# Kernel tuning notes

Measured on AMD Instinct MI355X. Metric: run time of the kernel, lower is better.

## Reference

```python
import jax, jax.numpy as jnp
import numpy as np

EPS = 1e-5  # BatchNorm eps


def _bn_relu(x, g, b, m, v):
    # inference-mode BatchNorm2d over channel axis 1, then ReLU
    inv = g / jnp.sqrt(v + EPS)
    return jax.nn.relu(x * inv[None, :, None, None] + (b - m * inv)[None, :, None, None])


def setup_inputs() -> dict:
    key = jax.random.key(0)
    ks = jax.random.split(key, 16)
    B, C, N, K = 8, 64, 16384, 16
    mlp = (128, 64, 64)
    inp = {
        "src_xyz": jax.random.normal(ks[0], (B, 3, N, K), jnp.float32),
        "tgt_xyz": jax.random.normal(ks[1], (B, 3, N), jnp.float32),
        "feature": jax.random.normal(ks[2], (B, C, N, K), jnp.float32),
    }
    prev = C + 4  # use_relation adds diff_xyz(3) + distance(1)
    i = 3
    for li, co in enumerate(mlp, 1):
        scale = (6.0 / (prev + co)) ** 0.5  # xavier_uniform
        inp[f"W{li}"] = jax.random.uniform(ks[i], (co, prev), jnp.float32, -scale, scale)
        inp[f"g{li}"] = jnp.ones((co,), jnp.float32)
        inp[f"b{li}"] = jnp.zeros((co,), jnp.float32)
        inp[f"m{li}"] = jnp.zeros((co,), jnp.float32)
        inp[f"v{li}"] = jnp.ones((co,), jnp.float32)
        prev = co
        i += 1
    return inp


def reference(src_xyz, tgt_xyz, feature,
              W1, g1, b1, m1, v1,
              W2, g2, b2, m2, v2,
              W3, g3, b3, m3, v3):
    d = 3  # NOTE: original code slices the NEIGHBOR dim to :3 (faithful quirk)
    diff = src_xyz[:, :, :, :d] - tgt_xyz[:, :, :, None]      # (B,3,N,3)
    dist = jnp.sum(diff * diff, axis=1, keepdims=True)        # (B,1,N,3)
    x = jnp.concatenate([feature[:, :, :, :d], diff, dist], axis=1)  # (B,C+4,N,3)
    for (W, g, b, m, v) in ((W1, g1, b1, m1, v1), (W2, g2, b2, m2, v2), (W3, g3, b3, m3, v3)):
        x = jnp.einsum('oc,bcnk->bonk', W, x)  # 1x1 conv (shared MLP)
        x = _bn_relu(x, g, b, m, v)
    return jnp.sum(x, axis=3)  # reduction='sum' over neighbor dim -> (B,64,N)
```

## Files before the change

### kernel.cpp

```cpp
#include <hip/hip_runtime.h>


typedef __attribute__((ext_vector_type(8))) short short8v;
typedef __attribute__((ext_vector_type(4))) float f32x4;

#define BN_EPS 1e-5f

__device__ __forceinline__ unsigned short f2bf(float f) {
    union { float f; unsigned u; } U; U.f = f;
    unsigned r = U.u + 0x7FFFu + ((U.u >> 16) & 1u);
    return (unsigned short)(r >> 16);
}

union FragU { uint4 u; short8v s; uint2 h[2]; };


__global__ __launch_bounds__(256) void fa_pack(
    const float* __restrict__ W1, const float* __restrict__ g1, const float* __restrict__ b1,
    const float* __restrict__ m1, const float* __restrict__ v1,
    const float* __restrict__ W2, const float* __restrict__ g2, const float* __restrict__ b2,
    const float* __restrict__ m2, const float* __restrict__ v2,
    const float* __restrict__ W3, const float* __restrict__ g3, const float* __restrict__ b3,
    const float* __restrict__ m3, const float* __restrict__ v3,
    char* __restrict__ ws)
{
    const int id = blockIdx.x * 256 + threadIdx.x;
    if (id < 1536) {
        const int lane = id & 63, frag = id >> 6;
        const int ct = frag / 3, ks = frag - 3 * ct;
        const int o  = ct * 16 + (lane & 15);
        const int kb = ks * 32 + (lane >> 4) * 8;
        unsigned short h[8];
        #pragma unroll
        for (int j = 0; j < 8; ++j) {
            const int k = kb + j;
            h[j] = (k < 68) ? f2bf(W1[o * 68 + k]) : (unsigned short)0;
        }
        uint4 pk;
        pk.x = h[0] | (h[1] << 16); pk.y = h[2] | (h[3] << 16);
        pk.z = h[4] | (h[5] << 16); pk.w = h[6] | (h[7] << 16);
        ((uint4*)ws)[id] = pk;
    } else if (id < 2560) {
        const int i2 = id - 1536;
        const int lane = i2 & 63, frag = i2 >> 6;
        const int o  = (frag >> 2) * 16 + (lane & 15);
        const int kb = (frag & 3) * 32 + (lane >> 4) * 8;
        unsigned short h[8];
        #pragma unroll
        for (int j = 0; j < 8; ++j) h[j] = f2bf(W2[o * 128 + kb + j]);
        uint4 pk;
        pk.x = h[0] | (h[1] << 16); pk.y = h[2] | (h[3] << 16);
        pk.z = h[4] | (h[5] << 16); pk.w = h[6] | (h[7] << 16);
        ((uint4*)(ws + 24576))[i2] = pk;
    } else if (id < 3072) {
        const int i3 = id - 2560;
        const int lane = i3 & 63, frag = i3 >> 6;
        const int o  = (frag >> 1) * 16 + (lane & 15);
        const int kb = (frag & 1) * 32 + (lane >> 4) * 8;
        unsigned short h[8];
        #pragma unroll
        for (int j = 0; j < 8; ++j) h[j] = f2bf(W3[o * 64 + kb + j]);
        uint4 pk;
        pk.x = h[0] | (h[1] << 16); pk.y = h[2] | (h[3] << 16);
        pk.z = h[4] | (h[5] << 16); pk.w = h[6] | (h[7] << 16);
        ((uint4*)(ws + 40960))[i3] = pk;
    } else if (id < 3200) {
        const int o = id - 3072;
        const float s = g1[o] * rsqrtf(v1[o] + BN_EPS);
        ((float*)(ws + 49152))[o] = s;
        ((float*)(ws + 49664))[o] = b1[o] - m1[o] * s;
    } else if (id < 3264) {
        const int o = id - 3200;
        const float s = g2[o] * rsqrtf(v2[o] + BN_EPS);
        ((float*)(ws + 50176))[o] = s;
        ((float*)(ws + 50432))[o] = b2[o] - m2[o] * s;
    } else if (id < 3328) {
        const int o = id - 3264;
        const float s = g3[o] * rsqrtf(v3[o] + BN_EPS);
        ((float*)(ws + 50688))[o] = s;
        ((float*)(ws + 50944))[o] = b3[o] - m3[o] * s;
    }
}

__global__ __launch_bounds__(128, 2) void fa_mfma(
    const float* __restrict__ src, const float* __restrict__ tgt,
    const float* __restrict__ feat,
    const char* __restrict__ ws, float* __restrict__ out)
{
    constexpr int N = 16384;
    __shared__ unsigned short X0[96 * 72];
    __shared__ unsigned short X1[96 * 136];

    const int t  = threadIdx.x;
    const int b  = blockIdx.x >> 9;
    const int n0 = (blockIdx.x & 511) << 5;

    {
        const int p  = t & 31;
        const int cg = t >> 5;
        #pragma unroll
        for (int it = 0; it < 4; ++it) {
            const int c0 = it * 16 + cg * 4;
            const float* fp = feat + ((size_t)(b * 64 + c0) * N + n0 + p) * 16;
            const float4 f0 = *(const float4*)(fp);
            const float4 f1 = *(const float4*)(fp + (size_t)N * 16);
            const float4 f2 = *(const float4*)(fp + (size_t)N * 32);
            const float4 f3 = *(const float4*)(fp + (size_t)N * 48);
            uint2 u0, u1, u2;
            u0.x = f2bf(f0.x) | (f2bf(f1.x) << 16); u0.y = f2bf(f2.x) | (f2bf(f3.x) << 16);
            u1.x = f2bf(f0.y) | (f2bf(f1.y) << 16); u1.y = f2bf(f2.y) | (f2bf(f3.y) << 16);
            u2.x = f2bf(f0.z) | (f2bf(f1.z) << 16); u2.y = f2bf(f2.z) | (f2bf(f3.z) << 16);
            *(uint2*)&X0[(0 * 32 + p) * 72 + c0] = u0;
            *(uint2*)&X0[(1 * 32 + p) * 72 + c0] = u1;
            *(uint2*)&X0[(2 * 32 + p) * 72 + c0] = u2;
        }
    }
    if (t < 96) {
        const int p = t & 31, k = t >> 5;
        const int n = n0 + p;
        const float d0 = src[((b * 3 + 0) * N + n) * 16 + k] - tgt[(b * 3 + 0) * N + n];
        const float d1 = src[((b * 3 + 1) * N + n) * 16 + k] - tgt[(b * 3 + 1) * N + n];
        const float d2 = src[((b * 3 + 2) * N + n) * 16 + k] - tgt[(b * 3 + 2) * N + n];
        const float ds = d0 * d0 + d1 * d1 + d2 * d2;
        uint2 wr; wr.x = f2bf(d0) | (f2bf(d1) << 16); wr.y = f2bf(d2) | (f2bf(ds) << 16);
        *(uint2*)&X0[(k * 32 + p) * 72 + 64] = wr;
        uint2 z; z.x = 0; z.y = 0;
        *(uint2*)&X0[(k * 32 + p) * 72 + 68] = z;
    }
    __syncthreads();

    const int w = t >> 6, lane = t & 63, lo = lane & 15, hi = lane >> 4;

    const uint4*  w1f = (const uint4*)ws;
    const uint4*  w2f = (const uint4*)(ws + 24576);
    const uint4*  w3f = (const uint4*)(ws + 40960);
    const float*  s1w = (const float*)(ws + 49152);
    const float*  t1w = (const float*)(ws + 49664);
    const float*  s2w = (const float*)(ws + 50176);
    const float*  t2w = (const float*)(ws + 50432);
    const float*  s3w = (const float*)(ws + 50688);
    const float*  t3w = (const float*)(ws + 50944);

    short8v a1[3][3];
    #pragma unroll
    for (int k = 0; k < 3; ++k) {
        const int row = k * 32 + w * 16 + lo;
        a1[k][0] = *(const short8v*)&X0[row * 72 + hi * 8];
        a1[k][1] = *(const short8v*)&X0[row * 72 + 32 + hi * 8];
        short8v az = {0, 0, 0, 0, 0, 0, 0, 0};
        if (hi == 0) {
            FragU U; U.s = az;
            U.h[0] = *(const uint2*)&X0[row * 72 + 64];
            az = U.s;
        }
        a1[k][2] = az;
    }
    #pragma unroll 2
    for (int ct = 0; ct < 8; ++ct) {
        FragU B0, B1, B2;
        B0.u = w1f[(ct * 3 + 0) * 64 + lane];
        B1.u = w1f[(ct * 3 + 1) * 64 + lane];
        B2.u = w1f[(ct * 3 + 2) * 64 + lane];
        const float sc = s1w[ct * 16 + lo];
        const float tb = t1w[ct * 16 + lo];
        #pragma unroll
        for (int k = 0; k < 3; ++k) {
            f32x4 acc = {0.f, 0.f, 0.f, 0.f};
            acc = __builtin_amdgcn_mfma_f32_16x16x32_bf16(a1[k][0], B0.s, acc, 0, 0, 0);
            acc = __builtin_amdgcn_mfma_f32_16x16x32_bf16(a1[k][1], B1.s, acc, 0, 0, 0);
            acc = __builtin_amdgcn_mfma_f32_16x16x32_bf16(a1[k][2], B2.s, acc, 0, 0, 0);
            const int rb = k * 32 + w * 16 + 4 * hi;
            #pragma unroll
            for (int j = 0; j < 4; ++j) {
                const float y = fmaxf(fmaf(sc, acc[j], tb), 0.f);
                X1[(rb + j) * 136 + ct * 16 + lo] = f2bf(y);
            }
        }
    }

    short8v a2[3][4];
    #pragma unroll
    for (int k = 0; k < 3; ++k) {
        const int row = k * 32 + w * 16 + lo;
        #pragma unroll
        for (int ks = 0; ks < 4; ++ks)
            a2[k][ks] = *(const short8v*)&X1[row * 136 + ks * 32 + hi * 8];
    }
    #pragma unroll 2
    for (int ct = 0; ct < 4; ++ct) {
        FragU B0, B1, B2, B3;
        B0.u = w2f[(ct * 4 + 0) * 64 + lane];
        B1.u = w2f[(ct * 4 + 1) * 64 + lane];
        B2.u = w2f[(ct * 4 + 2) * 64 + lane];
        B3.u = w2f[(ct * 4 + 3) * 64 + lane];
        const float sc = s2w[ct * 16 + lo];
        const float tb = t2w[ct * 16 + lo];
        #pragma unroll
        for (int k = 0; k < 3; ++k) {
            f32x4 acc = {0.f, 0.f, 0.f, 0.f};
            acc = __builtin_amdgcn_mfma_f32_16x16x32_bf16(a2[k][0], B0.s, acc, 0, 0, 0);
            acc = __builtin_amdgcn_mfma_f32_16x16x32_bf16(a2[k][1], B1.s, acc, 0, 0, 0);
            acc = __builtin_amdgcn_mfma_f32_16x16x32_bf16(a2[k][2], B2.s, acc, 0, 0, 0);
            acc = __builtin_amdgcn_mfma_f32_16x16x32_bf16(a2[k][3], B3.s, acc, 0, 0, 0);
            const int rb = k * 32 + w * 16 + 4 * hi;
            #pragma unroll
            for (int j = 0; j < 4; ++j) {
                const float y = fmaxf(fmaf(sc, acc[j], tb), 0.f);
                X0[(rb + j) * 72 + ct * 16 + lo] = f2bf(y);
            }
        }
    }

    short8v a3[3][2];
    #pragma unroll
    for (int k = 0; k < 3; ++k) {
        const int row = k * 32 + w * 16 + lo;
        a3[k][0] = *(const short8v*)&X0[row * 72 + hi * 8];
        a3[k][1] = *(const short8v*)&X0[row * 72 + 32 + hi * 8];
    }
    #pragma unroll 2
    for (int ct = 0; ct < 4; ++ct) {
        FragU B0, B1;
        B0.u = w3f[(ct * 2 + 0) * 64 + lane];
        B1.u = w3f[(ct * 2 + 1) * 64 + lane];
        const float sc = s3w[ct * 16 + lo];
        const float tb = t3w[ct * 16 + lo];
        f32x4 acc0 = {0.f, 0.f, 0.f, 0.f};
        f32x4 acc1 = {0.f, 0.f, 0.f, 0.f};
        f32x4 acc2 = {0.f, 0.f, 0.f, 0.f};
        acc0 = __builtin_amdgcn_mfma_f32_16x16x32_bf16(a3[0][0], B0.s, acc0, 0, 0, 0);
        acc0 = __builtin_amdgcn_mfma_f32_16x16x32_bf16(a3[0][1], B1.s, acc0, 0, 0, 0);
        acc1 = __builtin_amdgcn_mfma_f32_16x16x32_bf16(a3[1][0], B0.s, acc1, 0, 0, 0);
        acc1 = __builtin_amdgcn_mfma_f32_16x16x32_bf16(a3[1][1], B1.s, acc1, 0, 0, 0);
        acc2 = __builtin_amdgcn_mfma_f32_16x16x32_bf16(a3[2][0], B0.s, acc2, 0, 0, 0);
        acc2 = __builtin_amdgcn_mfma_f32_16x16x32_bf16(a3[2][1], B1.s, acc2, 0, 0, 0);
        float4 r;
        float* rp = &r.x;
        #pragma unroll
        for (int j = 0; j < 4; ++j) {
            rp[j] = fmaxf(fmaf(sc, acc0[j], tb), 0.f)
                  + fmaxf(fmaf(sc, acc1[j], tb), 0.f)
                  + fmaxf(fmaf(sc, acc2[j], tb), 0.f);
        }
        float* op = out + (size_t)(b * 64 + ct * 16 + lo) * N + n0 + w * 16 + 4 * hi;
        *(float4*)op = r;
    }
}

extern "C" void kernel_launch(void* const* d_in, const int* in_sizes, int n_in,
                              void* d_out, int out_size, void* d_ws, size_t ws_size,
                              hipStream_t stream)
{
    const float* src  = (const float*)d_in[0];
    const float* tgt  = (const float*)d_in[1];
    const float* feat = (const float*)d_in[2];
    const float* W1 = (const float*)d_in[3];
    const float* g1 = (const float*)d_in[4];
    const float* b1 = (const float*)d_in[5];
    const float* m1 = (const float*)d_in[6];
    const float* v1 = (const float*)d_in[7];
    const float* W2 = (const float*)d_in[8];
    const float* g2 = (const float*)d_in[9];
    const float* b2 = (const float*)d_in[10];
    const float* m2 = (const float*)d_in[11];
    const float* v2 = (const float*)d_in[12];
    const float* W3 = (const float*)d_in[13];
    const float* g3 = (const float*)d_in[14];
    const float* b3 = (const float*)d_in[15];
    const float* m3 = (const float*)d_in[16];
    const float* v3 = (const float*)d_in[17];
    float* out = (float*)d_out;
    char* ws = (char*)d_ws;

    hipLaunchKernelGGL(fa_pack, dim3(13), dim3(256), 0, stream,
                       W1, g1, b1, m1, v1, W2, g2, b2, m2, v2, W3, g3, b3, m3, v3, ws);
    hipLaunchKernelGGL(fa_mfma, dim3(8 * 512), dim3(128), 0, stream,
                       src, tgt, feat, ws, out);
}
```

Measured before the change: 144.1 us.

## Alias LDS buffers, batch global loads up front, raise occupancy to three blocks

The two shared-memory staging buffers are merged into one aliased array, with extra barriers so each layer's fragments are read into registers before the buffer is overwritten. This cuts LDS use per block. The launch bound is raised to ask for three blocks per SIMD. All 16 feature float4 loads and the src/tgt loads are now issued before any conversion, to expose more memory-level parallelism. The trade-offs are higher register pressure from the 16 buffered float4 values, which may conflict with the tighter register budget, and two added block-wide barriers. The zero padding write at column 68 is also dropped, since those entries are never read.

```diff
diff --git a/kernel.cpp b/kernel.cpp
--- a/kernel.cpp
+++ b/kernel.cpp
@@ -82,14 +82,15 @@
     }
 }
 
-__global__ __launch_bounds__(128, 2) void fa_mfma(
+__global__ __launch_bounds__(128, 3) void fa_mfma(
     const float* __restrict__ src, const float* __restrict__ tgt,
     const float* __restrict__ feat,
     const char* __restrict__ ws, float* __restrict__ out)
 {
     constexpr int N = 16384;
-    __shared__ unsigned short X0[96 * 72];
-    __shared__ unsigned short X1[96 * 136];
+    __shared__ unsigned short SM[96 * 136];
+    #define X0V(r, c) SM[(r) * 72 + (c)]
+    #define X1V(r, c) SM[(r) * 136 + (c)]
 
     const int t  = threadIdx.x;
     const int b  = blockIdx.x >> 9;
@@ -98,34 +99,42 @@
     {
         const int p  = t & 31;
         const int cg = t >> 5;
+        float4 fr[16];
+        #pragma unroll
+        for (int it = 0; it < 4; ++it) {
+            const float* fp = feat + ((size_t)(b * 64 + it * 16 + cg * 4) * N + n0 + p) * 16;
+            #pragma unroll
+            for (int q = 0; q < 4; ++q)
+                fr[it * 4 + q] = *(const float4*)(fp + (size_t)q * N * 16);
+        }
+        float rs0 = 0, rs1 = 0, rs2 = 0, rt0 = 0, rt1 = 0, rt2 = 0;
+        const bool rel = t < 96;
+        const int rp = t & 31, rk = t >> 5;
+        if (rel) {
+            const int n = n0 + rp;
+            rs0 = src[((b * 3 + 0) * N + n) * 16 + rk]; rt0 = tgt[(b * 3 + 0) * N + n];
+            rs1 = src[((b * 3 + 1) * N + n) * 16 + rk]; rt1 = tgt[(b * 3 + 1) * N + n];
+            rs2 = src[((b * 3 + 2) * N + n) * 16 + rk]; rt2 = tgt[(b * 3 + 2) * N + n];
+        }
         #pragma unroll
         for (int it = 0; it < 4; ++it) {
             const int c0 = it * 16 + cg * 4;
-            const float* fp = feat + ((size_t)(b * 64 + c0) * N + n0 + p) * 16;
-            const float4 f0 = *(const float4*)(fp);
-            const float4 f1 = *(const float4*)(fp + (size_t)N * 16);
-            const float4 f2 = *(const float4*)(fp + (size_t)N * 32);
-            const float4 f3 = *(const float4*)(fp + (size_t)N * 48);
+            const float4 f0 = fr[it * 4 + 0], f1 = fr[it * 4 + 1];
+            const float4 f2 = fr[it * 4 + 2], f3 = fr[it * 4 + 3];
             uint2 u0, u1, u2;
             u0.x = f2bf(f0.x) | (f2bf(f1.x) << 16); u0.y = f2bf(f2.x) | (f2bf(f3.x) << 16);
             u1.x = f2bf(f0.y) | (f2bf(f1.y) << 16); u1.y = f2bf(f2.y) | (f2bf(f3.y) << 16);
             u2.x = f2bf(f0.z) | (f2bf(f1.z) << 16); u2.y = f2bf(f2.z) | (f2bf(f3.z) << 16);
-            *(uint2*)&X0[(0 * 32 + p) * 72 + c0] = u0;
-            *(uint2*)&X0[(1 * 32 + p) * 72 + c0] = u1;
-            *(uint2*)&X0[(2 * 32 + p) * 72 + c0] = u2;
-        }
-    }
-    if (t < 96) {
-        const int p = t & 31, k = t >> 5;
-        const int n = n0 + p;
-        const float d0 = src[((b * 3 + 0) * N + n) * 16 + k] - tgt[(b * 3 + 0) * N + n];
-        const float d1 = src[((b * 3 + 1) * N + n) * 16 + k] - tgt[(b * 3 + 1) * N + n];
-        const float d2 = src[((b * 3 + 2) * N + n) * 16 + k] - tgt[(b * 3 + 2) * N + n];
-        const float ds = d0 * d0 + d1 * d1 + d2 * d2;
-        uint2 wr; wr.x = f2bf(d0) | (f2bf(d1) << 16); wr.y = f2bf(d2) | (f2bf(ds) << 16);
-        *(uint2*)&X0[(k * 32 + p) * 72 + 64] = wr;
-        uint2 z; z.x = 0; z.y = 0;
-        *(uint2*)&X0[(k * 32 + p) * 72 + 68] = z;
+            *(uint2*)&X0V(0 * 32 + p, c0) = u0;
+            *(uint2*)&X0V(1 * 32 + p, c0) = u1;
+            *(uint2*)&X0V(2 * 32 + p, c0) = u2;
+        }
+        if (rel) {
+            const float d0 = rs0 - rt0, d1 = rs1 - rt1, d2 = rs2 - rt2;
+            const float ds = d0 * d0 + d1 * d1 + d2 * d2;
+            uint2 wr; wr.x = f2bf(d0) | (f2bf(d1) << 16); wr.y = f2bf(d2) | (f2bf(ds) << 16);
+            *(uint2*)&X0V(rk * 32 + rp, 64) = wr;
+        }
     }
     __syncthreads();
 
@@ -145,16 +154,14 @@
     #pragma unroll
     for (int k = 0; k < 3; ++k) {
         const int row = k * 32 + w * 16 + lo;
-        a1[k][0] = *(const short8v*)&X0[row * 72 + hi * 8];
-        a1[k][1] = *(const short8v*)&X0[row * 72 + 32 + hi * 8];
-        short8v az = {0, 0, 0, 0, 0, 0, 0, 0};
-        if (hi == 0) {
-            FragU U; U.s = az;
-            U.h[0] = *(const uint2*)&X0[row * 72 + 64];
-            az = U.s;
-        }
-        a1[k][2] = az;
-    }
+        a1[k][0] = *(const short8v*)&X0V(row, hi * 8);
+        a1[k][1] = *(const short8v*)&X0V(row, 32 + hi * 8);
+        FragU U; U.u.x = 0; U.u.y = 0; U.u.z = 0; U.u.w = 0;
+        if (hi == 0) U.h[0] = *(const uint2*)&X0V(row, 64);
+        a1[k][2] = U.s;
+    }
+    __syncthreads();
+
     #pragma unroll 2
     for (int ct = 0; ct < 8; ++ct) {
         FragU B0, B1, B2;
@@ -173,7 +180,7 @@
             #pragma unroll
             for (int j = 0; j < 4; ++j) {
                 const float y = fmaxf(fmaf(sc, acc[j], tb), 0.f);
-                X1[(rb + j) * 136 + ct * 16 + lo] = f2bf(y);
+                X1V(rb + j, ct * 16 + lo) = f2bf(y);
             }
         }
     }
@@ -184,8 +191,10 @@
         const int row = k * 32 + w * 16 + lo;
         #pragma unroll
         for (int ks = 0; ks < 4; ++ks)
-            a2[k][ks] = *(const short8v*)&X1[row * 136 + ks * 32 + hi * 8];
-    }
+            a2[k][ks] = *(const short8v*)&X1V(row, ks * 32 + hi * 8);
+    }
+    __syncthreads();
+
     #pragma unroll 2
     for (int ct = 0; ct < 4; ++ct) {
         FragU B0, B1, B2, B3;
@@ -206,7 +215,7 @@
             #pragma unroll
             for (int j = 0; j < 4; ++j) {
                 const float y = fmaxf(fmaf(sc, acc[j], tb), 0.f);
-                X0[(rb + j) * 72 + ct * 16 + lo] = f2bf(y);
+                X0V(rb + j, ct * 16 + lo) = f2bf(y);
             }
         }
     }
@@ -215,8 +224,8 @@
     #pragma unroll
     for (int k = 0; k < 3; ++k) {
         const int row = k * 32 + w * 16 + lo;
-        a3[k][0] = *(const short8v*)&X0[row * 72 + hi * 8];
-        a3[k][1] = *(const short8v*)&X0[row * 72 + 32 + hi * 8];
+        a3[k][0] = *(const short8v*)&X0V(row, hi * 8);
+        a3[k][1] = *(const short8v*)&X0V(row, 32 + hi * 8);
     }
     #pragma unroll 2
     for (int ct = 0; ct < 4; ++ct) {
@@ -245,6 +254,8 @@
         float* op = out + (size_t)(b * 64 + ct * 16 + lo) * N + n0 + w * 16 + 4 * hi;
         *(float4*)op = r;
     }
+    #undef X0V
+    #undef X1V
 }
 
 extern "C" void kernel_launch(void* const* d_in, const int* in_sizes, int n_in,
```

Result: faster. 136.7 us (-5.1%).
